# Performance work log

Measured on AMD Instinct MI355X. Metric: run time of the kernel, lower is better.

## Reference

```python
import jax, jax.numpy as jnp
import numpy as np

B, NS, S, H = 2048, 8, 8, 512   # batch, num_units, num_mem_slots, hidden==num_mem_size
WH, WK = 1, 32                  # write attention heads, key_size
RH, RK = 4, 32                  # read (mem) attention heads, mem_attention_key


def _lin(x, W, b):
    # torch nn.Linear convention: W is [out, in]
    return jnp.einsum('...i,oi->...o', x, W) + b


def setup_inputs() -> dict:
    key = jax.random.key(0)
    ks = jax.random.split(key, 13)
    def w(k, o, i):
        return jax.random.normal(k, (o, i), jnp.float32) * 0.02
    d = {
        'h_s': jax.random.normal(ks[0], (B, NS, H), jnp.float32),
        'mem': jax.random.normal(ks[1], (B, S, H), jnp.float32),
        'wq_w': w(ks[2], WH * WK, H), 'wq_b': jnp.zeros((WH * WK,), jnp.float32),
        'wk_w': w(ks[3], WH * WK, H), 'wk_b': jnp.zeros((WH * WK,), jnp.float32),
        'wv_w': w(ks[4], WH * H, H), 'wv_b': jnp.zeros((WH * H,), jnp.float32),
        'wo_w': w(ks[5], H, WH * H), 'wo_b': jnp.zeros((H,), jnp.float32),
        'ut_w': w(ks[6], H, H),      'ut_b': jnp.zeros((H,), jnp.float32),
        'ug_w': w(ks[7], 2 * H, H),  'ug_b': jnp.zeros((2 * H,), jnp.float32),
        'rq_w': w(ks[8], RH * RK, H), 'rq_b': jnp.zeros((RH * RK,), jnp.float32),
        'rk_w': w(ks[9], RH * RK, H), 'rk_b': jnp.zeros((RH * RK,), jnp.float32),
        'rv_w': w(ks[10], RH * H, H), 'rv_b': jnp.zeros((RH * H,), jnp.float32),
        'ro_w': w(ks[11], H, RH * H), 'ro_b': jnp.zeros((H,), jnp.float32),
    }
    return d


def _forward(h_s, mem, wq_w, wq_b, wk_w, wk_b, wv_w, wv_b, wo_w, wo_b,
             ut_w, ut_b, ug_w, ug_b, rq_w, rq_b, rk_w, rk_b, rv_w, rv_b,
             ro_w, ro_b):
    b = h_s.shape[0]
    T = NS + S  # concat length for write keys/values

    # ---------------- write ----------------
    xi = jnp.concatenate([h_s, mem], axis=1)                       # [B, T, H]
    q = _lin(mem, wq_w, wq_b).reshape(b, S, WH, WK).transpose(0, 2, 1, 3)   # [B,WH,S,WK]
    k = _lin(xi, wk_w, wk_b).reshape(b, T, WH, WK).transpose(0, 2, 1, 3)    # [B,WH,T,WK]
    v = _lin(xi, wv_w, wv_b).reshape(b, T, WH, H).transpose(0, 2, 1, 3)     # [B,WH,T,H]
    scores = jnp.einsum('bhsk,bhtk->bhst', q, k) / np.sqrt(WK).astype(np.float32)
    probs = jax.nn.softmax(scores, axis=-1)                         # [B,WH,S,T]
    ctx = jnp.einsum('bhst,bhtd->bhsd', probs, v)                   # [B,WH,S,H]
    ctx = ctx.transpose(0, 2, 1, 3).reshape(b, S, WH * H)
    mem_write = _lin(ctx, wo_w, wo_b)                               # [B,S,H]

    # ---------------- update (GRU-like gating) ----------------
    inputs_mean = jax.nn.relu(_lin(h_s, ut_w, ut_b)).mean(axis=1, keepdims=True)  # [B,1,H]
    kk = inputs_mean + jnp.tanh(mem)                                # [B,S,H]
    gates = jax.nn.sigmoid(_lin(kk, ug_w, ug_b))                    # [B,S,2H]
    input_gate, forget_gate = gates[..., :H], gates[..., H:]
    mem_new = input_gate * jnp.tanh(mem_write) + forget_gate * mem  # [B,S,H]

    # ---------------- read ----------------
    q = _lin(h_s, rq_w, rq_b).reshape(b, NS, RH, RK).transpose(0, 2, 1, 3)      # [B,RH,NS,RK]
    k = _lin(mem_new, rk_w, rk_b).reshape(b, S, RH, RK).transpose(0, 2, 1, 3)   # [B,RH,S,RK]
    v = _lin(mem_new, rv_w, rv_b).reshape(b, S, RH, H).transpose(0, 2, 1, 3)    # [B,RH,S,H]
    scores = jnp.einsum('bhnk,bhsk->bhns', q, k) / np.sqrt(RK).astype(np.float32)
    probs = jax.nn.softmax(scores, axis=-1)                          # [B,RH,NS,S]
    ctx = jnp.einsum('bhns,bhsd->bhnd', probs, v)                    # [B,RH,NS,H]
    ctx = ctx.transpose(0, 2, 1, 3).reshape(b, NS, RH * H)
    h_out = h_s + _lin(ctx, ro_w, ro_b)                              # residual
    return h_out, mem_new


def reference(h_s, mem, wq_w, wq_b, wk_w, wk_b, wv_w, wv_b, wo_w, wo_b,
              ut_w, ut_b, ug_w, ug_b, rq_w, rq_b, rk_w, rk_b, rv_w, rv_b,
              ro_w, ro_b):
    return _forward(h_s, mem, wq_w, wq_b, wk_w, wk_b, wv_w, wv_b, wo_w, wo_b,
                    ut_w, ut_b, ug_w, ug_b, rq_w, rq_b, rk_w, rk_b, rv_w, rv_b,
                    ro_w, ro_b)
```

## Files before the change

### kernel.cpp

```cpp
#include <hip/hip_runtime.h>

#define Bb   2048
#define Mrows 16384
#define Hd   512

typedef float  f32x4  __attribute__((ext_vector_type(4)));
typedef __bf16 bf16x8 __attribute__((ext_vector_type(8)));
typedef unsigned short us8 __attribute__((ext_vector_type(8)));

__device__ __forceinline__ unsigned short f2bf(float f) {
    unsigned int u = __builtin_bit_cast(unsigned int, f);
    u = u + 0x7FFFu + ((u >> 16) & 1u);
    return (unsigned short)(u >> 16);
}
__device__ __forceinline__ float bf2f(unsigned short h) {
    unsigned int u = ((unsigned int)h) << 16;
    return __builtin_bit_cast(float, u);
}

__device__ __forceinline__ void gload_lds16(const unsigned short* g, void* lds) {
    __builtin_amdgcn_global_load_lds(
        (const __attribute__((address_space(1))) unsigned int*)g,
        (__attribute__((address_space(3))) unsigned int*)lds,
        16, 0, 0);
}

#define MB (1024ull*1024ull)
#define OFF_WQ   0ull
#define OFF_WK   32768ull
#define OFF_WV   65536ull
#define OFF_WO   589824ull
#define OFF_UT   1114112ull
#define OFF_UG   1638400ull
#define OFF_RQ   2686976ull
#define OFF_RK   2818048ull
#define OFF_RV   2949120ull
#define OFF_RO   5046272ull
#define OFF_HS    (8*MB)
#define OFF_MEM   (24*MB)
#define OFF_UTR   (40*MB)
#define OFF_MEAN  (56*MB)
#define OFF_Q1    (60*MB)
#define OFF_K1    (62*MB)
#define OFF_V1    (66*MB)
#define OFF_CTX1  (100*MB)
#define OFF_KK    (116*MB)
#define OFF_TMW   (132*MB)
#define OFF_GATES (148*MB)
#define OFF_MNB   (180*MB)
#define OFF_Q2    (196*MB)
#define OFF_K2    (204*MB)
#define OFF_RVO   (40*MB)
#define OFF_CTX2  (104*MB)

struct CastSeg { const float* src; unsigned short* dst; int n4; };
struct CastParams { CastSeg seg[12]; };

__global__ __launch_bounds__(256) void cast_all(CastParams p) {
    CastSeg s = p.seg[blockIdx.y];
    int stride = gridDim.x * blockDim.x;
    for (int i = blockIdx.x * blockDim.x + threadIdx.x; i < s.n4; i += stride) {
        float4 v = reinterpret_cast<const float4*>(s.src)[i];
        ushort4 o;
        o.x = f2bf(v.x); o.y = f2bf(v.y); o.z = f2bf(v.z); o.w = f2bf(v.w);
        reinterpret_cast<ushort4*>(s.dst)[i] = o;
    }
}

template<int MODE>
__device__ __forceinline__ void store_c(void* out, const float* extra, int row,
                                        int col, int ldo, int remap_off, float v) {
    if (MODE == 0) {
        ((float*)out)[(size_t)row * ldo + col] = v;
    } else if (MODE == 1) {
        ((unsigned short*)out)[(size_t)row * ldo + col] = f2bf(v);
    } else if (MODE == 2) {
        ((unsigned short*)out)[(size_t)row * ldo + col] = f2bf(fmaxf(v, 0.f));
    } else if (MODE == 3) {
        ((unsigned short*)out)[(size_t)row * ldo + col] = f2bf(1.f / (1.f + expf(-v)));
    } else if (MODE == 4) {
        ((unsigned short*)out)[(size_t)row * ldo + col] = f2bf(tanhf(v));
    } else if (MODE == 5) {
        int rr = ((row >> 3) << 4) + (row & 7) + remap_off;
        ((float*)out)[(size_t)rr * ldo + col] = v;
    } else if (MODE == 6) {
        int rr = ((row >> 3) << 4) + (row & 7) + remap_off;
        ((unsigned short*)out)[(size_t)rr * ldo + col] = f2bf(v);
    } else if (MODE == 7) {
        ((float*)out)[(size_t)row * ldo + col] = v + extra[(size_t)row * ldo + col];
    }
}

template<int K, int MODE>
__global__ __launch_bounds__(256) void gemm_big(
    const unsigned short* __restrict__ A, const unsigned short* __restrict__ W,
    const float* __restrict__ bias, void* __restrict__ out,
    const float* __restrict__ extra, int N, int ldo, int remap_off)
{
    constexpr int NT = K / 64;
    __shared__ __align__(16) unsigned short As[128 * 64];
    __shared__ __align__(16) unsigned short Bs[128 * 64];

    const int nwg = (int)gridDim.x;
    const int swz = ((int)blockIdx.x & 7) * (nwg >> 3) + ((int)blockIdx.x >> 3);
    const int tiles_n = N >> 7;
    const int bm = swz / tiles_n;
    const int bn = swz - bm * tiles_n;

    const int t = threadIdx.x;
    const int wave = t >> 6, lane = t & 63;
    const int wr = (wave >> 1) * 64;
    const int wc = (wave & 1) * 64;
    const int lrow = lane & 15;
    const int lkh  = lane >> 4;

    const unsigned short* ga[4];
    const unsigned short* gb[4];
    #pragma unroll
    for (int j = 0; j < 4; j++) {
        int c   = wave * 256 + j * 64 + lane;
        int row = c >> 3;
        int kl  = (c & 7) ^ (row & 7);
        ga[j] = A + (size_t)(bm * 128 + row) * K + kl * 8;
        gb[j] = W + (size_t)(bn * 128 + row) * K + kl * 8;
    }

    int aof[4][2], bof[4][2];
    #pragma unroll
    for (int m = 0; m < 4; m++) {
        int ra = wr + m * 16 + lrow;
        int rb = wc + m * 16 + lrow;
        #pragma unroll
        for (int kk = 0; kk < 2; kk++) {
            int kc = kk * 4 + lkh;
            aof[m][kk] = ra * 64 + ((kc ^ (ra & 7)) << 3);
            bof[m][kk] = rb * 64 + ((kc ^ (rb & 7)) << 3);
        }
    }

    f32x4 acc[4][4] = {};

    #pragma unroll
    for (int j = 0; j < 4; j++) {
        gload_lds16(ga[j], (char*)As + (wave * 4 + j) * 1024);
        gload_lds16(gb[j], (char*)Bs + (wave * 4 + j) * 1024);
    }

    for (int kt = 0; kt < NT; ++kt) {
        __syncthreads();
        #pragma unroll
        for (int kk = 0; kk < 2; kk++) {
            bf16x8 af[4], bf_[4];
            #pragma unroll
            for (int m = 0; m < 4; m++)
                af[m] = __builtin_bit_cast(bf16x8,
                            *reinterpret_cast<const us8*>(&As[aof[m][kk]]));
            #pragma unroll
            for (int n = 0; n < 4; n++)
                bf_[n] = __builtin_bit_cast(bf16x8,
                            *reinterpret_cast<const us8*>(&Bs[bof[n][kk]]));
            #pragma unroll
            for (int m = 0; m < 4; m++)
                #pragma unroll
                for (int n = 0; n < 4; n++)
                    acc[m][n] = __builtin_amdgcn_mfma_f32_16x16x32_bf16(
                                    af[m], bf_[n], acc[m][n], 0, 0, 0);
        }
        __syncthreads();
        if (kt + 1 < NT) {
            #pragma unroll
            for (int j = 0; j < 4; j++) {
                gload_lds16(ga[j] + (kt + 1) * 64, (char*)As + (wave * 4 + j) * 1024);
                gload_lds16(gb[j] + (kt + 1) * 64, (char*)Bs + (wave * 4 + j) * 1024);
            }
        }
    }

    #pragma unroll
    for (int n = 0; n < 4; n++) {
        int col = bn * 128 + wc + n * 16 + lrow;
        float bv = bias[col];
        #pragma unroll
        for (int m = 0; m < 4; m++) {
            #pragma unroll
            for (int r = 0; r < 4; r++) {
                int row = bm * 128 + wr + m * 16 + lkh * 4 + r;
                store_c<MODE>(out, extra, row, col, ldo, remap_off,
                              acc[m][n][r] + bv);
            }
        }
    }
}

template<int TN, int MODE, int K>
__global__ __launch_bounds__(256) void gemm_small(
    const unsigned short* __restrict__ A, const unsigned short* __restrict__ W,
    const float* __restrict__ bias, void* __restrict__ out,
    const float* __restrict__ extra, int N, int ldo, int remap_off)
{
    constexpr int BN = 16 * TN;
    const int tiles_n = N / BN;
    const int bm = blockIdx.x / tiles_n;
    const int bn = blockIdx.x % tiles_n;
    const int wave = threadIdx.x >> 6;
    const int lane = threadIdx.x & 63;
    const int row0 = bm * 64 + wave * 16;
    const int col0 = bn * BN;
    const int lrow = lane & 15;
    const int lk   = (lane >> 4) << 3;

    f32x4 acc[TN] = {};
    const unsigned short* ap  = A + (size_t)(row0 + lrow) * K + lk;
    const unsigned short* wp0 = W + (size_t)(col0 + lrow) * K + lk;

    #pragma unroll 4
    for (int ks = 0; ks < K; ks += 32) {
        bf16x8 af = __builtin_bit_cast(bf16x8,
                        *reinterpret_cast<const us8*>(ap + ks));
        #pragma unroll
        for (int tt = 0; tt < TN; tt++) {
            bf16x8 bfm = __builtin_bit_cast(bf16x8,
                        *reinterpret_cast<const us8*>(wp0 + (size_t)tt * 16 * K + ks));
            acc[tt] = __builtin_amdgcn_mfma_f32_16x16x32_bf16(af, bfm, acc[tt], 0, 0, 0);
        }
    }

    #pragma unroll
    for (int tt = 0; tt < TN; tt++) {
        int col = col0 + tt * 16 + lrow;
        float bv = bias[col];
        #pragma unroll
        for (int r = 0; r < 4; r++) {
            int row = row0 + (lane >> 4) * 4 + r;
            store_c<MODE>(out, extra, row, col, ldo, remap_off, acc[tt][r] + bv);
        }
    }
}

__global__ __launch_bounds__(256) void mean_kernel(
    const unsigned short* __restrict__ UTR, float* __restrict__ MEAN)
{
    int idx = blockIdx.x * blockDim.x + threadIdx.x;
    if (idx >= Bb * Hd) return;
    int b = idx >> 9, j = idx & 511;
    float s = 0.f;
    #pragma unroll
    for (int r = 0; r < 8; r++)
        s += bf2f(UTR[((size_t)(b * 8 + r) << 9) + j]);
    MEAN[idx] = s * 0.125f;
}

__global__ __launch_bounds__(256) void kk_kernel(
    const float* __restrict__ MEAN, const float* __restrict__ mem,
    unsigned short* __restrict__ KK)
{
    int idx = blockIdx.x * blockDim.x + threadIdx.x;
    int m = idx >> 9;
    int bj = ((m >> 3) << 9) + (idx & 511);
    KK[idx] = f2bf(MEAN[bj] + tanhf(mem[idx]));
}

__global__ __launch_bounds__(256) void memnew_kernel(
    const unsigned short* __restrict__ GATES, const unsigned short* __restrict__ TMW,
    const float* __restrict__ mem, float* __restrict__ out_mem,
    unsigned short* __restrict__ MNB)
{
    int idx = blockIdx.x * blockDim.x + threadIdx.x;
    int m = idx >> 9, j = idx & 511;
    float ig = bf2f(GATES[(size_t)m * 1024 + j]);
    float fg = bf2f(GATES[(size_t)m * 1024 + 512 + j]);
    float v  = ig * bf2f(TMW[idx]) + fg * mem[idx];
    out_mem[idx] = v;
    MNB[idx] = f2bf(v);
}

__global__ __launch_bounds__(256) void attn1_kernel(
    const float* __restrict__ Q1, const float* __restrict__ K1,
    const unsigned short* __restrict__ V1, unsigned short* __restrict__ CTX1)
{
    int b = blockIdx.x, t = threadIdx.x;
    __shared__ float q[8][32], k[16][32], pr[8][16];
    q[t >> 5][t & 31] = Q1[(size_t)b * 256 + t];
    k[t >> 5][t & 31]       = K1[(size_t)b * 512 + t];
    k[8 + (t >> 5)][t & 31] = K1[(size_t)b * 512 + 256 + t];
    __syncthreads();
    if (t < 128) {
        int s = t >> 4, tt = t & 15;
        float acc = 0.f;
        #pragma unroll
        for (int i = 0; i < 32; i++) acc += q[s][i] * k[tt][i];
        pr[s][tt] = acc * 0.17677669529663687f;
    }
    __syncthreads();
    if (t < 8) {
        float m = -1e30f;
        for (int i = 0; i < 16; i++) m = fmaxf(m, pr[t][i]);
        float e[16], sum = 0.f;
        for (int i = 0; i < 16; i++) { e[i] = expf(pr[t][i] - m); sum += e[i]; }
        float inv = 1.f / sum;
        for (int i = 0; i < 16; i++) pr[t][i] = e[i] * inv;
    }
    __syncthreads();
    int s = t >> 5, d0 = (t & 31) * 16;
    float a[16];
    #pragma unroll
    for (int i = 0; i < 16; i++) a[i] = 0.f;
    for (int tt = 0; tt < 16; tt++) {
        float p = pr[s][tt];
        const unsigned short* vp = V1 + ((size_t)(b * 16 + tt)) * 512 + d0;
        us8 v0 = *reinterpret_cast<const us8*>(vp);
        us8 v1 = *reinterpret_cast<const us8*>(vp + 8);
        #pragma unroll
        for (int i = 0; i < 8; i++) a[i]     += p * bf2f(v0[i]);
        #pragma unroll
        for (int i = 0; i < 8; i++) a[8 + i] += p * bf2f(v1[i]);
    }
    us8 o0, o1;
    #pragma unroll
    for (int i = 0; i < 8; i++) { o0[i] = f2bf(a[i]); o1[i] = f2bf(a[8 + i]); }
    unsigned short* cp = CTX1 + ((size_t)(b * 8 + s)) * 512 + d0;
    *reinterpret_cast<us8*>(cp) = o0;
    *reinterpret_cast<us8*>(cp + 8) = o1;
}

__global__ __launch_bounds__(256) void attn2_kernel(
    const float* __restrict__ Q2, const float* __restrict__ K2,
    const unsigned short* __restrict__ V2, unsigned short* __restrict__ CTX2)
{
    int b = blockIdx.x, t = threadIdx.x;
    __shared__ float q[8][128], k[8][128], pr[4][8][8];
    for (int i = t; i < 1024; i += 256) {
        q[i >> 7][i & 127] = Q2[(size_t)b * 1024 + i];
        k[i >> 7][i & 127] = K2[(size_t)b * 1024 + i];
    }
    __syncthreads();
    {
        int h = t >> 6, n = (t >> 3) & 7, s = t & 7;
        float acc = 0.f;
        #pragma unroll
        for (int i = 0; i < 32; i++) acc += q[n][h * 32 + i] * k[s][h * 32 + i];
        pr[h][n][s] = acc * 0.17677669529663687f;
    }
    __syncthreads();
    if (t < 32) {
        int h = t >> 3, n = t & 7;
        float m = -1e30f;
        for (int i = 0; i < 8; i++) m = fmaxf(m, pr[h][n][i]);
        float e[8], sum = 0.f;
        for (int i = 0; i < 8; i++) { e[i] = expf(pr[h][n][i] - m); sum += e[i]; }
        float inv = 1.f / sum;
        for (int i = 0; i < 8; i++) pr[h][n][i] = e[i] * inv;
    }
    __syncthreads();
    int n = t >> 5, d0 = (t & 31) * 16;
    for (int h = 0; h < 4; h++) {
        float a[16];
        #pragma unroll
        for (int i = 0; i < 16; i++) a[i] = 0.f;
        for (int s = 0; s < 8; s++) {
            float p = pr[h][n][s];
            const unsigned short* vp = V2 + ((size_t)(b * 8 + s)) * 2048 + h * 512 + d0;
            us8 v0 = *reinterpret_cast<const us8*>(vp);
            us8 v1 = *reinterpret_cast<const us8*>(vp + 8);
            #pragma unroll
            for (int i = 0; i < 8; i++) a[i]     += p * bf2f(v0[i]);
            #pragma unroll
            for (int i = 0; i < 8; i++) a[8 + i] += p * bf2f(v1[i]);
        }
        us8 o0, o1;
        #pragma unroll
        for (int i = 0; i < 8; i++) { o0[i] = f2bf(a[i]); o1[i] = f2bf(a[8 + i]); }
        unsigned short* cp = CTX2 + ((size_t)(b * 8 + n)) * 2048 + h * 512 + d0;
        *reinterpret_cast<us8*>(cp) = o0;
        *reinterpret_cast<us8*>(cp + 8) = o1;
    }
}

extern "C" void kernel_launch(void* const* d_in, const int* in_sizes, int n_in,
                              void* d_out, int out_size, void* d_ws, size_t ws_size,
                              hipStream_t stream)
{
    const float* h_s  = (const float*)d_in[0];
    const float* mem  = (const float*)d_in[1];
    const float* wq_w = (const float*)d_in[2];  const float* wq_b = (const float*)d_in[3];
    const float* wk_w = (const float*)d_in[4];  const float* wk_b = (const float*)d_in[5];
    const float* wv_w = (const float*)d_in[6];  const float* wv_b = (const float*)d_in[7];
    const float* wo_w = (const float*)d_in[8];  const float* wo_b = (const float*)d_in[9];
    const float* ut_w = (const float*)d_in[10]; const float* ut_b = (const float*)d_in[11];
    const float* ug_w = (const float*)d_in[12]; const float* ug_b = (const float*)d_in[13];
    const float* rq_w = (const float*)d_in[14]; const float* rq_b = (const float*)d_in[15];
    const float* rk_w = (const float*)d_in[16]; const float* rk_b = (const float*)d_in[17];
    const float* rv_w = (const float*)d_in[18]; const float* rv_b = (const float*)d_in[19];
    const float* ro_w = (const float*)d_in[20]; const float* ro_b = (const float*)d_in[21];

    char* ws = (char*)d_ws;
    unsigned short* WQb = (unsigned short*)(ws + OFF_WQ);
    unsigned short* WKb = (unsigned short*)(ws + OFF_WK);
    unsigned short* WVb = (unsigned short*)(ws + OFF_WV);
    unsigned short* WOb = (unsigned short*)(ws + OFF_WO);
    unsigned short* UTb = (unsigned short*)(ws + OFF_UT);
    unsigned short* UGb = (unsigned short*)(ws + OFF_UG);
    unsigned short* RQb = (unsigned short*)(ws + OFF_RQ);
    unsigned short* RKb = (unsigned short*)(ws + OFF_RK);
    unsigned short* RVb = (unsigned short*)(ws + OFF_RV);
    unsigned short* ROb = (unsigned short*)(ws + OFF_RO);
    unsigned short* HSb  = (unsigned short*)(ws + OFF_HS);
    unsigned short* MEMb = (unsigned short*)(ws + OFF_MEM);
    unsigned short* UTR  = (unsigned short*)(ws + OFF_UTR);
    float*          MEAN = (float*)(ws + OFF_MEAN);
    float*          Q1   = (float*)(ws + OFF_Q1);
    float*          K1   = (float*)(ws + OFF_K1);
    unsigned short* V1   = (unsigned short*)(ws + OFF_V1);
    unsigned short* CTX1 = (unsigned short*)(ws + OFF_CTX1);
    unsigned short* KKb  = (unsigned short*)(ws + OFF_KK);
    unsigned short* TMW  = (unsigned short*)(ws + OFF_TMW);
    unsigned short* GATES= (unsigned short*)(ws + OFF_GATES);
    unsigned short* MNB  = (unsigned short*)(ws + OFF_MNB);
    float*          Q2   = (float*)(ws + OFF_Q2);
    float*          K2   = (float*)(ws + OFF_K2);
    unsigned short* RVO  = (unsigned short*)(ws + OFF_RVO);
    unsigned short* CTX2 = (unsigned short*)(ws + OFF_CTX2);

    float* out   = (float*)d_out;
    float* out_m = out + (size_t)Mrows * Hd;

    CastParams cp;
    cp.seg[0]  = { h_s,  HSb,  (Mrows * Hd) / 4 };
    cp.seg[1]  = { mem,  MEMb, (Mrows * Hd) / 4 };
    cp.seg[2]  = { wq_w, WQb,  (32 * 512) / 4 };
    cp.seg[3]  = { wk_w, WKb,  (32 * 512) / 4 };
    cp.seg[4]  = { wv_w, WVb,  (512 * 512) / 4 };
    cp.seg[5]  = { wo_w, WOb,  (512 * 512) / 4 };
    cp.seg[6]  = { ut_w, UTb,  (512 * 512) / 4 };
    cp.seg[7]  = { ug_w, UGb,  (1024 * 512) / 4 };
    cp.seg[8]  = { rq_w, RQb,  (128 * 512) / 4 };
    cp.seg[9]  = { rk_w, RKb,  (128 * 512) / 4 };
    cp.seg[10] = { rv_w, RVb,  (2048 * 512) / 4 };
    cp.seg[11] = { ro_w, ROb,  (512 * 2048) / 4 };
    cast_all<<<dim3(2048, 12), 256, 0, stream>>>(cp);

    gemm_big<512,2><<<512,  256, 0, stream>>>(HSb,  UTb, ut_b, UTR, nullptr, 512, 512, 0);
    gemm_big<512,0><<<128,  256, 0, stream>>>(HSb,  RQb, rq_b, Q2,  nullptr, 128, 128, 0);
    gemm_small<2,5,512><<<256, 256, 0, stream>>>(HSb, WKb, wk_b, K1, nullptr, 32, 32, 0);
    gemm_big<512,6><<<512,  256, 0, stream>>>(HSb,  WVb, wv_b, V1,  nullptr, 512, 512, 0);
    gemm_small<2,0,512><<<256, 256, 0, stream>>>(MEMb, WQb, wq_b, Q1, nullptr, 32, 32, 0);
    gemm_small<2,5,512><<<256, 256, 0, stream>>>(MEMb, WKb, wk_b, K1, nullptr, 32, 32, 8);
    gemm_big<512,6><<<512,  256, 0, stream>>>(MEMb, WVb, wv_b, V1,  nullptr, 512, 512, 8);

    mean_kernel<<<4096, 256, 0, stream>>>(UTR, MEAN);
    kk_kernel<<<32768, 256, 0, stream>>>(MEAN, mem, KKb);

    attn1_kernel<<<Bb, 256, 0, stream>>>(Q1, K1, V1, CTX1);

    gemm_big<512,4><<<512,  256, 0, stream>>>(CTX1, WOb, wo_b, TMW,   nullptr,  512,  512, 0);
    gemm_big<512,3><<<1024, 256, 0, stream>>>(KKb,  UGb, ug_b, GATES, nullptr, 1024, 1024, 0);

    memnew_kernel<<<32768, 256, 0, stream>>>(GATES, TMW, mem, out_m, MNB);

    gemm_big<512,0><<<128,  256, 0, stream>>>(MNB, RKb, rk_b, K2,  nullptr,  128,  128, 0);
    gemm_big<512,1><<<2048, 256, 0, stream>>>(MNB, RVb, rv_b, RVO, nullptr, 2048, 2048, 0);

    attn2_kernel<<<Bb, 256, 0, stream>>>(Q2, K2, RVO, CTX2);

    gemm_big<2048,7><<<512, 256, 0, stream>>>(CTX2, ROb, ro_b, out, h_s, 512, 512, 0);

    (void)in_sizes; (void)n_in; (void)out_size; (void)ws_size;
}
```

Before: 516.5 us.

## Batch independent GEMMs into grouped launches and double-buffer LDS tiles

Replaces the per-GEMM gemm_big launches with a gemm_multi kernel that takes up to four segments, so several independent GEMMs sharing a launch run in one grid. Segment choice and epilogue mode are resolved at runtime. The K loop now double-buffers the A/B tiles in LDS, issuing the next tile's global-to-LDS loads before computing the current one, with one barrier per iteration. This aims to cut launch overhead and tail underutilisation and to overlap memory loads with MFMA work. In exchange it doubles LDS use per block (occupancy hint of 2) and adds a runtime switch over epilogue modes.

Measured after the change: 532.5 us. +3.1%, slower.

```diff
diff --git a/kernel.cpp b/kernel.cpp
--- a/kernel.cpp
+++ b/kernel.cpp
@@ -91,21 +91,35 @@
     }
 }
 
-template<int K, int MODE>
-__global__ __launch_bounds__(256) void gemm_big(
-    const unsigned short* __restrict__ A, const unsigned short* __restrict__ W,
-    const float* __restrict__ bias, void* __restrict__ out,
-    const float* __restrict__ extra, int N, int ldo, int remap_off)
+struct GemmSeg {
+    const unsigned short* A;
+    const unsigned short* W;
+    const float* bias;
+    void* out;
+    const float* extra;
+    int mode, ldo, remap_off, tile0;
+};
+struct GemmParams { GemmSeg seg[4]; int nseg; int tiles_tot; };
+
+template<int K>
+__global__ __launch_bounds__(256, 2) void gemm_multi(GemmParams p)
 {
     constexpr int NT = K / 64;
-    __shared__ __align__(16) unsigned short As[128 * 64];
-    __shared__ __align__(16) unsigned short Bs[128 * 64];
+    __shared__ __align__(16) unsigned short As[2][128 * 64];
+    __shared__ __align__(16) unsigned short Bs[2][128 * 64];
 
     const int nwg = (int)gridDim.x;
     const int swz = ((int)blockIdx.x & 7) * (nwg >> 3) + ((int)blockIdx.x >> 3);
-    const int tiles_n = N >> 7;
-    const int bm = swz / tiles_n;
-    const int bn = swz - bm * tiles_n;
+    const int bm = swz / p.tiles_tot;
+    const int tl = swz - bm * p.tiles_tot;
+
+    int si = 0;
+    #pragma unroll
+    for (int i = 1; i < 4; i++)
+        if (i < p.nseg && tl >= p.seg[i].tile0) si = i;
+    const unsigned short* Aseg = p.seg[si].A;
+    const unsigned short* Wseg = p.seg[si].W;
+    const int bn = tl - p.seg[si].tile0;
 
     const int t = threadIdx.x;
     const int wave = t >> 6, lane = t & 63;
@@ -121,8 +135,8 @@
         int c   = wave * 256 + j * 64 + lane;
         int row = c >> 3;
         int kl  = (c & 7) ^ (row & 7);
-        ga[j] = A + (size_t)(bm * 128 + row) * K + kl * 8;
-        gb[j] = W + (size_t)(bn * 128 + row) * K + kl * 8;
+        ga[j] = Aseg + (size_t)(bm * 128 + row) * K + kl * 8;
+        gb[j] = Wseg + (size_t)(bn * 128 + row) * K + kl * 8;
     }
 
     int aof[4][2], bof[4][2];
@@ -142,23 +156,32 @@
 
     #pragma unroll
     for (int j = 0; j < 4; j++) {
-        gload_lds16(ga[j], (char*)As + (wave * 4 + j) * 1024);
-        gload_lds16(gb[j], (char*)Bs + (wave * 4 + j) * 1024);
-    }
-
+        gload_lds16(ga[j], (char*)As[0] + (wave * 4 + j) * 1024);
+        gload_lds16(gb[j], (char*)Bs[0] + (wave * 4 + j) * 1024);
+    }
+    __syncthreads();
+
+    #pragma unroll 8
     for (int kt = 0; kt < NT; ++kt) {
-        __syncthreads();
+        const int cur = kt & 1, nxt = cur ^ 1;
+        if (kt + 1 < NT) {
+            #pragma unroll
+            for (int j = 0; j < 4; j++) {
+                gload_lds16(ga[j] + (kt + 1) * 64, (char*)As[nxt] + (wave * 4 + j) * 1024);
+                gload_lds16(gb[j] + (kt + 1) * 64, (char*)Bs[nxt] + (wave * 4 + j) * 1024);
+            }
+        }
         #pragma unroll
         for (int kk = 0; kk < 2; kk++) {
             bf16x8 af[4], bf_[4];
             #pragma unroll
             for (int m = 0; m < 4; m++)
                 af[m] = __builtin_bit_cast(bf16x8,
-                            *reinterpret_cast<const us8*>(&As[aof[m][kk]]));
+                            *reinterpret_cast<const us8*>(&As[cur][aof[m][kk]]));
             #pragma unroll
             for (int n = 0; n < 4; n++)
                 bf_[n] = __builtin_bit_cast(bf16x8,
-                            *reinterpret_cast<const us8*>(&Bs[bof[n][kk]]));
+                            *reinterpret_cast<const us8*>(&Bs[cur][bof[n][kk]]));
             #pragma unroll
             for (int m = 0; m < 4; m++)
                 #pragma unroll
@@ -167,29 +190,39 @@
                                     af[m], bf_[n], acc[m][n], 0, 0, 0);
         }
         __syncthreads();
-        if (kt + 1 < NT) {
-            #pragma unroll
-            for (int j = 0; j < 4; j++) {
-                gload_lds16(ga[j] + (kt + 1) * 64, (char*)As + (wave * 4 + j) * 1024);
-                gload_lds16(gb[j] + (kt + 1) * 64, (char*)Bs + (wave * 4 + j) * 1024);
-            }
-        }
-    }
-
-    #pragma unroll
-    for (int n = 0; n < 4; n++) {
-        int col = bn * 128 + wc + n * 16 + lrow;
-        float bv = bias[col];
-        #pragma unroll
-        for (int m = 0; m < 4; m++) {
-            #pragma unroll
-            for (int r = 0; r < 4; r++) {
-                int row = bm * 128 + wr + m * 16 + lkh * 4 + r;
-                store_c<MODE>(out, extra, row, col, ldo, remap_off,
-                              acc[m][n][r] + bv);
-            }
-        }
-    }
+    }
+
+    void* outp = p.seg[si].out;
+    const float* bias = p.seg[si].bias;
+    const float* extra = p.seg[si].extra;
+    const int ldo = p.seg[si].ldo, rmo = p.seg[si].remap_off, mode = p.seg[si].mode;
+
+    #define EPI(MODE_)                                                          \
+        _Pragma("unroll")                                                       \
+        for (int n = 0; n < 4; n++) {                                           \
+            int col = bn * 128 + wc + n * 16 + lrow;                            \
+            float bv = bias[col];                                               \
+            _Pragma("unroll")                                                   \
+            for (int m = 0; m < 4; m++) {                                       \
+                _Pragma("unroll")                                               \
+                for (int r = 0; r < 4; r++) {                                   \
+                    int row = bm * 128 + wr + m * 16 + lkh * 4 + r;             \
+                    store_c<MODE_>(outp, extra, row, col, ldo, rmo,             \
+                                   acc[m][n][r] + bv);                          \
+                }                                                               \
+            }                                                                   \
+        }
+    switch (mode) {
+        case 0: EPI(0) break;
+        case 1: EPI(1) break;
+        case 2: EPI(2) break;
+        case 3: EPI(3) break;
+        case 4: EPI(4) break;
+        case 5: EPI(5) break;
+        case 6: EPI(6) break;
+        default: EPI(7) break;
+    }
+    #undef EPI
 }
 
 template<int TN, int MODE, int K>
@@ -439,30 +472,50 @@
     cp.seg[11] = { ro_w, ROb,  (512 * 2048) / 4 };
     cast_all<<<dim3(2048, 12), 256, 0, stream>>>(cp);
 
-    gemm_big<512,2><<<512,  256, 0, stream>>>(HSb,  UTb, ut_b, UTR, nullptr, 512, 512, 0);
-    gemm_big<512,0><<<128,  256, 0, stream>>>(HSb,  RQb, rq_b, Q2,  nullptr, 128, 128, 0);
-    gemm_small<2,5,512><<<256, 256, 0, stream>>>(HSb, WKb, wk_b, K1, nullptr, 32, 32, 0);
-    gemm_big<512,6><<<512,  256, 0, stream>>>(HSb,  WVb, wv_b, V1,  nullptr, 512, 512, 0);
+    {
+        GemmParams g;
+        g.seg[0] = { HSb,  UTb, ut_b, UTR, nullptr, 2, 512,  0, 0 };
+        g.seg[1] = { HSb,  WVb, wv_b, V1,  nullptr, 6, 512,  0, 4 };
+        g.seg[2] = { HSb,  RQb, rq_b, Q2,  nullptr, 0, 128,  0, 8 };
+        g.seg[3] = { MEMb, WVb, wv_b, V1,  nullptr, 6, 512,  8, 9 };
+        g.nseg = 4; g.tiles_tot = 13;
+        gemm_multi<512><<<128 * 13, 256, 0, stream>>>(g);
+    }
+    gemm_small<2,5,512><<<256, 256, 0, stream>>>(HSb,  WKb, wk_b, K1, nullptr, 32, 32, 0);
     gemm_small<2,0,512><<<256, 256, 0, stream>>>(MEMb, WQb, wq_b, Q1, nullptr, 32, 32, 0);
     gemm_small<2,5,512><<<256, 256, 0, stream>>>(MEMb, WKb, wk_b, K1, nullptr, 32, 32, 8);
-    gemm_big<512,6><<<512,  256, 0, stream>>>(MEMb, WVb, wv_b, V1,  nullptr, 512, 512, 8);
 
     mean_kernel<<<4096, 256, 0, stream>>>(UTR, MEAN);
     kk_kernel<<<32768, 256, 0, stream>>>(MEAN, mem, KKb);
 
     attn1_kernel<<<Bb, 256, 0, stream>>>(Q1, K1, V1, CTX1);
 
-    gemm_big<512,4><<<512,  256, 0, stream>>>(CTX1, WOb, wo_b, TMW,   nullptr,  512,  512, 0);
-    gemm_big<512,3><<<1024, 256, 0, stream>>>(KKb,  UGb, ug_b, GATES, nullptr, 1024, 1024, 0);
+    {
+        GemmParams g;
+        g.seg[0] = { CTX1, WOb, wo_b, TMW,   nullptr, 4,  512, 0, 0 };
+        g.seg[1] = { KKb,  UGb, ug_b, GATES, nullptr, 3, 1024, 0, 4 };
+        g.nseg = 2; g.tiles_tot = 12;
+        gemm_multi<512><<<128 * 12, 256, 0, stream>>>(g);
+    }
 
     memnew_kernel<<<32768, 256, 0, stream>>>(GATES, TMW, mem, out_m, MNB);
 
-    gemm_big<512,0><<<128,  256, 0, stream>>>(MNB, RKb, rk_b, K2,  nullptr,  128,  128, 0);
-    gemm_big<512,1><<<2048, 256, 0, stream>>>(MNB, RVb, rv_b, RVO, nullptr, 2048, 2048, 0);
+    {
+        GemmParams g;
+        g.seg[0] = { MNB, RKb, rk_b, K2,  nullptr, 0,  128, 0, 0 };
+        g.seg[1] = { MNB, RVb, rv_b, RVO, nullptr, 1, 2048, 0, 1 };
+        g.nseg = 2; g.tiles_tot = 17;
+        gemm_multi<512><<<128 * 17, 256, 0, stream>>>(g);
+    }
 
     attn2_kernel<<<Bb, 256, 0, stream>>>(Q2, K2, RVO, CTX2);
 
-    gemm_big<2048,7><<<512, 256, 0, stream>>>(CTX2, ROb, ro_b, out, h_s, 512, 512, 0);
+    {
+        GemmParams g;
+        g.seg[0] = { CTX2, ROb, ro_b, out, h_s, 7, 512, 0, 0 };
+        g.nseg = 1; g.tiles_tot = 4;
+        gemm_multi<2048><<<128 * 4, 256, 0, stream>>>(g);
+    }
 
     (void)in_sizes; (void)n_in; (void)out_size; (void)ws_size;
 }
```
